# Optimization experiments

Measured on AMD Instinct MI355X. Metric: run time of the kernel, lower is better.

Reference implementation:

```python
import jax, jax.numpy as jnp
import numpy as np

B, T, K, H = 4, 2048, 1024, 16
D = K // H

def setup_inputs() -> dict:
    key = jax.random.key(0)
    kx, kq, kk, kv = jax.random.split(key, 4)
    s = 1.0 / np.sqrt(K)
    return {
        "x": jax.random.normal(kx, (B, T, K), dtype=jnp.float32),
        "Wq": jax.random.normal(kq, (K, K), dtype=jnp.float32) * s,
        "Wk": jax.random.normal(kk, (K, K), dtype=jnp.float32) * s,
        "Wv": jax.random.normal(kv, (K, K), dtype=jnp.float32) * s,
    }

def reference(x, Wq, Wk, Wv):
    b, t, k = x.shape
    h, d = H, K // H
    # projections -> (b, h, t, d)
    q = (x @ Wq.T).reshape(b, t, h, d).transpose(0, 2, 1, 3)
    ke = (x @ Wk.T).reshape(b, t, h, d).transpose(0, 2, 1, 3)
    v = (x @ Wv.T).reshape(b, t, h, d).transpose(0, 2, 1, 3)
    scale = d ** (-0.25)  # applied to both q and k, as in the original
    scores = jnp.einsum('bhqd,bhkd->bhqk', q * scale, ke * scale)
    causal = jnp.triu(jnp.ones((t, t), dtype=bool), k=1)
    scores = jnp.where(causal, -jnp.inf, scores)
    attn = jax.nn.softmax(scores, axis=-1)
    out = jnp.einsum('bhqk,bhkd->bhqd', attn, v)
    return out.transpose(0, 2, 1, 3).reshape(b, t, k)
```

## Files before the change

### kernel.cpp

```cpp
#include <hip/hip_runtime.h>
#include <hip/hip_bf16.h>
#include <math.h>

#define B_   4
#define T_   2048
#define KDIM 1024
#define H_   16
#define D_   64
#define BH_  (B_*H_)
#define M_   (B_*T_)

typedef __bf16 bf16;
typedef __bf16 bf16x8 __attribute__((ext_vector_type(8)));
typedef __bf16 bf16x4 __attribute__((ext_vector_type(4)));
typedef float  f32x4  __attribute__((ext_vector_type(4)));
typedef float  f32x16 __attribute__((ext_vector_type(16)));
typedef unsigned int u32;
typedef u32 u32x4 __attribute__((ext_vector_type(4)));

static __device__ __forceinline__ f32x4 mfma16(bf16x8 a, bf16x8 b, f32x4 c) {
    return __builtin_amdgcn_mfma_f32_16x16x32_bf16(a, b, c, 0, 0, 0);
}
static __device__ __forceinline__ f32x16 mfma32(bf16x8 a, bf16x8 b, f32x16 c) {
    return __builtin_amdgcn_mfma_f32_32x32x16_bf16(a, b, c, 0, 0, 0);
}
static __device__ __forceinline__ float exp2_fast(float x) {
    float r; asm("v_exp_f32 %0, %1" : "=v"(r) : "v"(x)); return r;
}

__global__ void cvt_f32_to_bf16(const float* __restrict__ src, bf16* __restrict__ dst, int n4) {
    int i = blockIdx.x * blockDim.x + threadIdx.x;
    if (i >= n4) return;
    float4 v = reinterpret_cast<const float4*>(src)[i];
    bf16x4 o;
    o.x = (bf16)v.x; o.y = (bf16)v.y; o.z = (bf16)v.z; o.w = (bf16)v.w;
    reinterpret_cast<bf16x4*>(dst)[i] = o;
}

__global__ __launch_bounds__(256) void proj_gemm(
    const bf16* __restrict__ xb, const bf16* __restrict__ Wall,
    bf16* __restrict__ Qb, bf16* __restrict__ Kb, bf16* __restrict__ Vtb)
{
    __shared__ __align__(16) bf16 Asm[128*64];
    __shared__ __align__(16) bf16 Bsm[128*64];

    const int tid  = threadIdx.x;
    const int wid  = tid >> 6;
    const int lane = tid & 63;
    const int l15  = lane & 15, l4 = lane >> 4;
    const int wr = wid >> 1, wc = wid & 1;
    const int row0 = blockIdx.x * 128;
    const int col0 = blockIdx.y * 128;
    const int wz   = blockIdx.z;
    const bf16* Wp = Wall + (size_t)wz * KDIM * KDIM;

    f32x4 acc[4][4] = {};

    for (int kt = 0; kt < KDIM/64; ++kt) {
        const int k0 = kt * 64;
        __syncthreads();
#pragma unroll
        for (int i = 0; i < 4; ++i) {
            int chunk = i*256 + tid;
            int rr = chunk >> 3;
            int cc = (chunk & 7) * 8;
            const bf16* ga = xb + (size_t)(row0 + rr)*KDIM + k0 + cc;
            bf16* la = Asm + (size_t)(i*256 + wid*64)*8;
            __builtin_amdgcn_global_load_lds(
                (const __attribute__((address_space(1))) void*)ga,
                (__attribute__((address_space(3))) void*)la, 16, 0, 0);
        }
#pragma unroll
        for (int i = 0; i < 4; ++i) {
            int chunk = i*256 + tid;
            int rr = chunk >> 3;
            int cc = (chunk & 7) * 8;
            const bf16* gb = Wp + (size_t)(col0 + rr)*KDIM + k0 + cc;
            bf16* lb = Bsm + (size_t)(i*256 + wid*64)*8;
            __builtin_amdgcn_global_load_lds(
                (const __attribute__((address_space(1))) void*)gb,
                (__attribute__((address_space(3))) void*)lb, 16, 0, 0);
        }
        asm volatile("s_waitcnt vmcnt(0)" ::: "memory");
        __syncthreads();

#pragma unroll
        for (int kk = 0; kk < 2; ++kk) {
            bf16x8 af[4], bfr[4];
#pragma unroll
            for (int m = 0; m < 4; ++m)
                af[m] = *reinterpret_cast<const bf16x8*>(Asm + (wr*64 + m*16 + l15)*64 + kk*32 + l4*8);
#pragma unroll
            for (int n = 0; n < 4; ++n)
                bfr[n] = *reinterpret_cast<const bf16x8*>(Bsm + (wc*64 + n*16 + l15)*64 + kk*32 + l4*8);
#pragma unroll
            for (int m = 0; m < 4; ++m)
#pragma unroll
                for (int n = 0; n < 4; ++n)
                    acc[m][n] = mfma16(af[m], bfr[n], acc[m][n]);
        }
    }

    const float osc = (wz == 0) ? 0.18033688011112042f : 1.0f;
#pragma unroll
    for (int m = 0; m < 4; ++m)
#pragma unroll
        for (int n = 0; n < 4; ++n)
#pragma unroll
            for (int r = 0; r < 4; ++r) {
                int gi = row0 + wr*64 + m*16 + l4*4 + r;
                int gj = col0 + wc*64 + n*16 + l15;
                bf16 o = (bf16)(acc[m][n][r] * osc);
                int bb = gi >> 11, tt = gi & (T_-1);
                int hh = gj >> 6,  dd = gj & (D_-1);
                size_t bh = (size_t)bb*H_ + hh;
                if (wz == 0)      Qb [(bh*T_ + tt)*D_ + dd] = o;
                else if (wz == 1) Kb [(bh*T_ + tt)*D_ + dd] = o;
                else              Vtb[(bh*D_ + dd)*T_ + tt] = o;
            }
}

__global__ __launch_bounds__(256) void flash_attn3(
    const bf16* __restrict__ Qb, const bf16* __restrict__ Kb,
    const bf16* __restrict__ Vtb, float* __restrict__ out)
{
    __shared__ __align__(16) char Ksm[8192];
    __shared__ __align__(16) char Vsm[8192];

    const int tid  = threadIdx.x;
    const int wid  = tid >> 6;
    const int lane = tid & 63;
    const int l31  = lane & 31;
    const int hi   = lane >> 5;

    const int orig = blockIdx.x;
    const int wg   = (orig & 7) * 128 + (orig >> 3);
    const int bh   = wg >> 4;
    const int qblk = (15 - (wg & 15)) * 128;
    const int q0   = qblk + wid * 32;
    const int q_abs = q0 + l31;

    const bf16* qp = Qb + ((size_t)bh*T_ + q_abs)*D_ + hi*8;
    bf16x8 qf[4];
#pragma unroll
    for (int j = 0; j < 4; ++j)
        qf[j] = *reinterpret_cast<const bf16x8*>(qp + j*16);

    const bf16* kbase = Kb  + (size_t)bh*T_*D_;
    const bf16* vbase = Vtb + (size_t)bh*D_*T_;

    f32x16 o0 = {}; f32x16 o1 = {};
    float lsum = 0.f;

    const int my_nt  = (q0 + 31) >> 6;
    const int blk_nt = qblk/64 + 1;
    const int tmaskb = q_abs - 4*hi;

    const int r0 = tid >> 3,          r1 = (tid + 256) >> 3;
    const int e0 = (tid & 7) * 8,     e1 = e0;
    const u32 lds0 = (u32)((r0*128 + e0*2) ^ ((r0 & 7) << 4));
    const u32 lds1 = (u32)((r1*128 + e1*2) ^ ((r1 & 7) << 4));

    u32x4 kr0, kr1, vr0, vr1;
    auto issue = [&](int nt) {
        kr0 = *reinterpret_cast<const u32x4*>(kbase + ((size_t)(nt*64 + r0))*D_ + e0);
        kr1 = *reinterpret_cast<const u32x4*>(kbase + ((size_t)(nt*64 + r1))*D_ + e1);
        vr0 = *reinterpret_cast<const u32x4*>(vbase + (size_t)r0*T_ + nt*64 + e0);
        vr1 = *reinterpret_cast<const u32x4*>(vbase + (size_t)r1*T_ + nt*64 + e1);
    };
    issue(0);

    auto subtile = [&](int s, int kvb_abs, bool maskit, bf16x8& pA, bf16x8& pB) {
        f32x16 sacc = {};
        const int row = s*32 + l31;
        const int sw  = (row & 7) << 4;
#pragma unroll
        for (int j = 0; j < 4; ++j) {
            bf16x8 kf = *reinterpret_cast<const bf16x8*>(Ksm + ((row*128 + j*32 + hi*16) ^ sw));
            sacc = mfma32(kf, qf[j], sacc);
        }
        const int tlim = tmaskb - kvb_abs;
        float p[16];
#pragma unroll
        for (int r = 0; r < 16; ++r) {
            const int crow0 = (r & 3) + 8*(r >> 2);
            float sv = sacc[r];
            if (maskit) sv = (crow0 > tlim) ? -INFINITY : sv;
            p[r] = exp2_fast(sv);
        }
        {
            float a0 = p[0]+p[1],   a1 = p[2]+p[3],   a2 = p[4]+p[5],   a3 = p[6]+p[7];
            float a4 = p[8]+p[9],   a5 = p[10]+p[11], a6 = p[12]+p[13], a7 = p[14]+p[15];
            lsum += ((a0+a1) + (a2+a3)) + ((a4+a5) + (a6+a7));
        }
        u32 w[8];
#pragma unroll
        for (int i = 0; i < 8; ++i) {
            u32 wv;
            asm("v_cvt_pk_bf16_f32 %0, %1, %2" : "=v"(wv) : "v"(p[2*i]), "v"(p[2*i+1]));
            w[i] = wv;
        }
        u32 a0w = w[0], a2w = w[2];
        asm("v_permlane32_swap_b32 %0, %1" : "+v"(a0w), "+v"(a2w));
        u32 a1w = w[1], a3w = w[3];
        asm("v_permlane32_swap_b32 %0, %1" : "+v"(a1w), "+v"(a3w));
        u32 b0w = w[4], b2w = w[6];
        asm("v_permlane32_swap_b32 %0, %1" : "+v"(b0w), "+v"(b2w));
        u32 b1w = w[5], b3w = w[7];
        asm("v_permlane32_swap_b32 %0, %1" : "+v"(b1w), "+v"(b3w));
        u32x4 A0 = {a0w, a1w, a2w, a3w};
        u32x4 A1 = {b0w, b1w, b2w, b3w};
        pA = __builtin_bit_cast(bf16x8, A0);
        pB = __builtin_bit_cast(bf16x8, A1);
    };

    auto pv = [&](int ks, bf16x8 pf) {
        const int swv = (l31 & 7) << 4;
        const int colb = ks*32 + hi*16;
        bf16x8 v0 = *reinterpret_cast<const bf16x8*>(Vsm + ((l31*128 + colb) ^ swv));
        bf16x8 v1 = *reinterpret_cast<const bf16x8*>(Vsm + (((32 + l31)*128 + colb) ^ swv));
        o0 = mfma32(v0, pf, o0);
        o1 = mfma32(v1, pf, o1);
    };

    for (int nt = 0; nt <= blk_nt; ++nt) {
        __syncthreads();
        *reinterpret_cast<u32x4*>(Ksm + lds0) = kr0;
        *reinterpret_cast<u32x4*>(Ksm + lds1) = kr1;
        *reinterpret_cast<u32x4*>(Vsm + lds0) = vr0;
        *reinterpret_cast<u32x4*>(Vsm + lds1) = vr1;
        __syncthreads();
        if (nt < blk_nt) issue(nt + 1);

        if (nt <= my_nt) {
            const bool partial = (nt == my_nt);
            const int  nsub = (!partial || (q0 & 32)) ? 2 : 1;
            bf16x8 pA, pB;
            subtile(0, nt*64, partial, pA, pB);
            pv(0, pA);
            pv(1, pB);
            if (nsub == 2) {
                subtile(1, nt*64 + 32, partial, pA, pB);
                pv(2, pA);
                pv(3, pB);
            }
        }
    }

    lsum += __shfl_xor(lsum, 32);
    const float inv = 1.0f / lsum;
    const int bb = bh >> 4, hh = bh & 15;
    float* orow = out + ((size_t)bb*T_ + q_abs)*KDIM + hh*64 + hi*4;
#pragma unroll
    for (int g = 0; g < 4; ++g) {
        f32x4 v0, v1;
#pragma unroll
        for (int j = 0; j < 4; ++j) { v0[j] = o0[g*4+j]*inv; v1[j] = o1[g*4+j]*inv; }
        *reinterpret_cast<f32x4*>(orow + g*8)      = v0;
        *reinterpret_cast<f32x4*>(orow + 32 + g*8) = v1;
    }
}

extern "C" void kernel_launch(void* const* d_in, const int* in_sizes, int n_in,
                              void* d_out, int out_size, void* d_ws, size_t ws_size,
                              hipStream_t stream) {
    (void)in_sizes; (void)n_in; (void)out_size; (void)ws_size;
    const float* x  = (const float*)d_in[0];
    const float* Wq = (const float*)d_in[1];
    const float* Wk = (const float*)d_in[2];
    const float* Wv = (const float*)d_in[3];
    float* out = (float*)d_out;

    bf16* xb  = (bf16*)d_ws;
    bf16* Wb  = xb + (size_t)M_*KDIM;
    bf16* Qb  = Wb + (size_t)3*KDIM*KDIM;
    bf16* Kb  = Qb + (size_t)M_*KDIM;
    bf16* Vtb = Kb + (size_t)M_*KDIM;

    const int n4x = M_*KDIM/4;
    const int n4w = KDIM*KDIM/4;
    cvt_f32_to_bf16<<<(n4x+255)/256, 256, 0, stream>>>(x,  xb, n4x);
    cvt_f32_to_bf16<<<(n4w+255)/256, 256, 0, stream>>>(Wq, Wb,               n4w);
    cvt_f32_to_bf16<<<(n4w+255)/256, 256, 0, stream>>>(Wk, Wb + (size_t)KDIM*KDIM,   n4w);
    cvt_f32_to_bf16<<<(n4w+255)/256, 256, 0, stream>>>(Wv, Wb + (size_t)2*KDIM*KDIM, n4w);

    proj_gemm<<<dim3(M_/128, KDIM/128, 3), 256, 0, stream>>>(xb, Wb, Qb, Kb, Vtb);
    flash_attn3<<<dim3(BH_*16), 256, 0, stream>>>(Qb, Kb, Vtb, out);
}
```

Baseline: 181.1 us.

## Rewrite QKV projection GEMM with 256x128 tiles, double buffering and swizzled LDS

Replaces the 128x128 projection GEMM with a 512-thread, 256x128-tile kernel. It treats the three weight matrices as one 3072-wide matrix and launches a flat grid with a remapped block order aimed at L2 locality. K-tiles are double-buffered in LDS through global_load_lds, with partial vmcnt waits so loads overlap MFMA work. LDS addresses use an XOR swizzle and the MFMA block is wrapped in s_setprio. LDS use doubles, which may lower occupancy, and the hand-written waitcnt/barrier ordering must stay correct.

```diff
diff --git a/kernel.cpp b/kernel.cpp
--- a/kernel.cpp
+++ b/kernel.cpp
@@ -9,6 +9,7 @@
 #define D_   64
 #define BH_  (B_*H_)
 #define M_   (B_*T_)
+#define NKT  (KDIM/64)
 
 typedef __bf16 bf16;
 typedef __bf16 bf16x8 __attribute__((ext_vector_type(8)));
@@ -37,82 +38,127 @@
     reinterpret_cast<bf16x4*>(dst)[i] = o;
 }
 
-__global__ __launch_bounds__(256) void proj_gemm(
-    const bf16* __restrict__ xb, const bf16* __restrict__ Wall,
+__global__ __launch_bounds__(512) void proj_gemm256(
+    const bf16* __restrict__ xb, const bf16* __restrict__ Wflat,
     bf16* __restrict__ Qb, bf16* __restrict__ Kb, bf16* __restrict__ Vtb)
 {
-    __shared__ __align__(16) bf16 Asm[128*64];
-    __shared__ __align__(16) bf16 Bsm[128*64];
+    __shared__ __align__(16) char As[2][256*64*2];
+    __shared__ __align__(16) char Bs[2][128*64*2];
 
     const int tid  = threadIdx.x;
     const int wid  = tid >> 6;
     const int lane = tid & 63;
     const int l15  = lane & 15, l4 = lane >> 4;
-    const int wr = wid >> 1, wc = wid & 1;
-    const int row0 = blockIdx.x * 128;
-    const int col0 = blockIdx.y * 128;
-    const int wz   = blockIdx.z;
-    const bf16* Wp = Wall + (size_t)wz * KDIM * KDIM;
+    const int wavem = wid >> 1, waven = wid & 1;
+
+    const int orig = blockIdx.x;
+    const int wg   = (orig & 7) * 96 + (orig >> 3);
+    const int mblk = wg & 31, nblk = wg >> 5;
+    const int row0 = mblk * 256, col0 = nblk * 128;
+
+    const bf16* asrc[4];
+#pragma unroll
+    for (int q = 0; q < 4; ++q) {
+        int c   = q*512 + tid;
+        int rr  = c >> 3;
+        int cb  = (c & 7) * 16;
+        int cbs = cb ^ ((rr & 4) << 3);
+        asrc[q] = xb + (size_t)(row0 + rr)*KDIM + (cbs >> 1);
+    }
+    const bf16* bsrc[2];
+#pragma unroll
+    for (int q = 0; q < 2; ++q) {
+        int c   = q*512 + tid;
+        int rr  = c >> 3;
+        int cb  = (c & 7) * 16;
+        int cbs = cb ^ ((rr & 4) << 3);
+        bsrc[q] = Wflat + (size_t)(col0 + rr)*KDIM + (cbs >> 1);
+    }
+
+    auto stage = [&](int kt, int b) {
+        const int k0 = kt * 64;
+#pragma unroll
+        for (int q = 0; q < 4; ++q) {
+            char* la = As[b] + (q*512 + wid*64)*16;
+            __builtin_amdgcn_global_load_lds(
+                (const __attribute__((address_space(1))) void*)(asrc[q] + k0),
+                (__attribute__((address_space(3))) void*)la, 16, 0, 0);
+        }
+#pragma unroll
+        for (int q = 0; q < 2; ++q) {
+            char* lb = Bs[b] + (q*512 + wid*64)*16;
+            __builtin_amdgcn_global_load_lds(
+                (const __attribute__((address_space(1))) void*)(bsrc[q] + k0),
+                (__attribute__((address_space(3))) void*)lb, 16, 0, 0);
+        }
+    };
 
     f32x4 acc[4][4] = {};
 
-    for (int kt = 0; kt < KDIM/64; ++kt) {
-        const int k0 = kt * 64;
-        __syncthreads();
-#pragma unroll
-        for (int i = 0; i < 4; ++i) {
-            int chunk = i*256 + tid;
-            int rr = chunk >> 3;
-            int cc = (chunk & 7) * 8;
-            const bf16* ga = xb + (size_t)(row0 + rr)*KDIM + k0 + cc;
-            bf16* la = Asm + (size_t)(i*256 + wid*64)*8;
-            __builtin_amdgcn_global_load_lds(
-                (const __attribute__((address_space(1))) void*)ga,
-                (__attribute__((address_space(3))) void*)la, 16, 0, 0);
-        }
-#pragma unroll
-        for (int i = 0; i < 4; ++i) {
-            int chunk = i*256 + tid;
-            int rr = chunk >> 3;
-            int cc = (chunk & 7) * 8;
-            const bf16* gb = Wp + (size_t)(col0 + rr)*KDIM + k0 + cc;
-            bf16* lb = Bsm + (size_t)(i*256 + wid*64)*8;
-            __builtin_amdgcn_global_load_lds(
-                (const __attribute__((address_space(1))) void*)gb,
-                (__attribute__((address_space(3))) void*)lb, 16, 0, 0);
-        }
-        asm volatile("s_waitcnt vmcnt(0)" ::: "memory");
-        __syncthreads();
-
+    const int sw    = (l15 & 4) << 3;
+    const int arow  = (wavem*64 + l15) * 128;
+    const int brow  = (waven*64 + l15) * 128;
+
+    auto compute = [&](int b) {
+        const char* Ap = As[b];
+        const char* Bp = Bs[b];
 #pragma unroll
         for (int kk = 0; kk < 2; ++kk) {
+            const int cbk = (kk*64 + l4*16) ^ sw;
             bf16x8 af[4], bfr[4];
 #pragma unroll
             for (int m = 0; m < 4; ++m)
-                af[m] = *reinterpret_cast<const bf16x8*>(Asm + (wr*64 + m*16 + l15)*64 + kk*32 + l4*8);
+                af[m] = *reinterpret_cast<const bf16x8*>(Ap + arow + m*2048 + cbk);
 #pragma unroll
             for (int n = 0; n < 4; ++n)
-                bfr[n] = *reinterpret_cast<const bf16x8*>(Bsm + (wc*64 + n*16 + l15)*64 + kk*32 + l4*8);
+                bfr[n] = *reinterpret_cast<const bf16x8*>(Bp + brow + n*2048 + cbk);
+            __builtin_amdgcn_s_setprio(1);
 #pragma unroll
             for (int m = 0; m < 4; ++m)
 #pragma unroll
                 for (int n = 0; n < 4; ++n)
                     acc[m][n] = mfma16(af[m], bfr[n], acc[m][n]);
-        }
-    }
-
-    const float osc = (wz == 0) ? 0.18033688011112042f : 1.0f;
+            __builtin_amdgcn_s_setprio(0);
+        }
+    };
+
+    stage(0, 0);
+    stage(1, 1);
+
+    for (int t = 0; t < NKT - 1; ++t) {
+        const int b = t & 1;
+        asm volatile("s_waitcnt vmcnt(6)" ::: "memory");
+        __builtin_amdgcn_sched_barrier(0);
+        __builtin_amdgcn_s_barrier();
+        __builtin_amdgcn_sched_barrier(0);
+        compute(b);
+        asm volatile("s_waitcnt lgkmcnt(0)" ::: "memory");
+        __builtin_amdgcn_sched_barrier(0);
+        __builtin_amdgcn_s_barrier();
+        __builtin_amdgcn_sched_barrier(0);
+        if (t < NKT - 2) stage(t + 2, b);
+    }
+    asm volatile("s_waitcnt vmcnt(0)" ::: "memory");
+    __builtin_amdgcn_sched_barrier(0);
+    __builtin_amdgcn_s_barrier();
+    __builtin_amdgcn_sched_barrier(0);
+    compute((NKT - 1) & 1);
+
 #pragma unroll
     for (int m = 0; m < 4; ++m)
 #pragma unroll
         for (int n = 0; n < 4; ++n)
 #pragma unroll
             for (int r = 0; r < 4; ++r) {
-                int gi = row0 + wr*64 + m*16 + l4*4 + r;
-                int gj = col0 + wc*64 + n*16 + l15;
-                bf16 o = (bf16)(acc[m][n][r] * osc);
+                int gi = row0 + wavem*64 + m*16 + l4*4 + r;
+                int gj = col0 + waven*64 + n*16 + l15;
+                int wz  = gj >> 10;
+                int gjw = gj & 1023;
+                float v = acc[m][n][r];
+                if (wz == 0) v *= 0.18033688011112042f;
+                bf16 o = (bf16)v;
                 int bb = gi >> 11, tt = gi & (T_-1);
-                int hh = gj >> 6,  dd = gj & (D_-1);
+                int hh = gjw >> 6, dd = gjw & (D_-1);
                 size_t bh = (size_t)bb*H_ + hh;
                 if (wz == 0)      Qb [(bh*T_ + tt)*D_ + dd] = o;
                 else if (wz == 1) Kb [(bh*T_ + tt)*D_ + dd] = o;
@@ -173,10 +219,10 @@
     auto subtile = [&](int s, int kvb_abs, bool maskit, bf16x8& pA, bf16x8& pB) {
         f32x16 sacc = {};
         const int row = s*32 + l31;
-        const int sw  = (row & 7) << 4;
+        const int swk = (row & 7) << 4;
 #pragma unroll
         for (int j = 0; j < 4; ++j) {
-            bf16x8 kf = *reinterpret_cast<const bf16x8*>(Ksm + ((row*128 + j*32 + hi*16) ^ sw));
+            bf16x8 kf = *reinterpret_cast<const bf16x8*>(Ksm + ((row*128 + j*32 + hi*16) ^ swk));
             sacc = mfma32(kf, qf[j], sacc);
         }
         const int tlim = tmaskb - kvb_abs;
@@ -284,6 +330,6 @@
     cvt_f32_to_bf16<<<(n4w+255)/256, 256, 0, stream>>>(Wk, Wb + (size_t)KDIM*KDIM,   n4w);
     cvt_f32_to_bf16<<<(n4w+255)/256, 256, 0, stream>>>(Wv, Wb + (size_t)2*KDIM*KDIM, n4w);
 
-    proj_gemm<<<dim3(M_/128, KDIM/128, 3), 256, 0, stream>>>(xb, Wb, Qb, Kb, Vtb);
+    proj_gemm256<<<dim3(768), 512, 0, stream>>>(xb, Wb, Qb, Kb, Vtb);
     flash_attn3<<<dim3(BH_*16), 256, 0, stream>>>(Qb, Kb, Vtb, out);
 }
```

New measurement: 202.7 us. 11.9% more time.
